# Performance work log

Measured on AMD Instinct MI355X. Metric: run time of the kernel, lower is better.

The kernel has to match this reference:

```python
import jax, jax.numpy as jnp
import numpy as np

T, C, H, W, CI = 4, 64, 96, 96, 16
PS, WS, STR0 = 7, 21, 4
KS, KA = 100, 100
SCALE = 10.0


def conv1x1(x, w, b):
    # x: [T,C,H,W], w: [O,C]
    return jnp.einsum('tchw,oc->tohw', x, w) + b[None, :, None, None]


def unfold_clip(x, ps):
    # clipped-boundary unfold: [T,C,H,W] -> [T, H*W, C*ps*ps]
    t, c, h, w = x.shape
    d = jnp.arange(ps)
    ii = jnp.clip(jnp.arange(h)[:, None] + d[None, :], 0, h - 1)  # [H,ps]
    jj = jnp.clip(jnp.arange(w)[:, None] + d[None, :], 0, w - 1)  # [W,ps]
    p = x[:, :, ii]            # [T,C,H,ps,W]
    p = p[:, :, :, :, jj]      # [T,C,H,ps,W,ps]
    p = jnp.transpose(p, (0, 2, 4, 1, 3, 5))  # [T,H,W,C,ps,ps]
    return p.reshape(t, h * w, c * ps * ps)


def setup_inputs() -> dict:
    key = jax.random.key(0)
    ks = jax.random.split(key, 9)
    s = lambda fan: 1.0 / np.sqrt(fan)
    return {
        'vid': jax.random.normal(ks[0], (T, C, H, W), jnp.float32),
        'g_w': jax.random.normal(ks[1], (CI, C), jnp.float32) * s(C),
        'g_b': jax.random.normal(ks[2], (CI,), jnp.float32) * 0.01,
        'theta_w': jax.random.normal(ks[3], (CI, C), jnp.float32) * s(C),
        'theta_b': jax.random.normal(ks[4], (CI,), jnp.float32) * 0.01,
        'phi_w': jax.random.normal(ks[5], (CI, C), jnp.float32) * s(C),
        'phi_b': jax.random.normal(ks[6], (CI,), jnp.float32) * 0.01,
        'W_w': jax.random.normal(ks[7], (C, CI), jnp.float32) * s(CI),
        'W_b': jax.random.normal(ks[8], (C,), jnp.float32) * 0.01,
    }


def reference(vid, g_w, g_b, theta_w, theta_b, phi_w, phi_b, W_w, W_b):
    t, c, h, w = vid.shape
    b1 = conv1x1(vid, g_w, g_b)          # query features  (g)
    b2 = conv1x1(vid, theta_w, theta_b)  # value features  (theta)
    b3 = conv1x1(vid, phi_w, phi_b)      # key features    (phi)

    b1u = unfold_clip(b1, PS)  # [T,HW,D]
    b2u = unfold_clip(b2, PS)
    b3u = unfold_clip(b3, PS)

    # query grid (stride0)
    qi, qj = jnp.meshgrid(jnp.arange(0, h, STR0), jnp.arange(0, w, STR0), indexing='ij')
    qi, qj = qi.reshape(-1), qj.reshape(-1)
    nq = qi.shape[0]
    qflat = qi * w + qj
    b1q = b1u[:, qflat]  # [T,nq,D]

    # centered spatial search window (stride1=1), clipped bounds
    off = jnp.arange(WS) - WS // 2
    ci = jnp.clip(qi[:, None] + off[None, :], 0, h - 1)  # [nq,WS]
    cj = jnp.clip(qj[:, None] + off[None, :], 0, w - 1)
    cand = (ci[:, :, None] * w + cj[:, None, :]).reshape(nq, WS * WS)

    # patch inner-product dists, one window offset at a time (memory-lean)
    def score(cidx):  # cidx: [nq]
        return jnp.einsum('tqd,tqd->tq', b1q, b3u[:, cidx])
    dists = jax.lax.map(score, cand.T)           # [WS*WS,T,nq]
    dists = jnp.transpose(dists, (1, 2, 0))      # [T,nq,WS*WS]

    vals, idx = jax.lax.top_k(dists, KS)
    vals, idx = vals[..., :KA], idx[..., :KA]
    yi = jax.nn.softmax(vals * SCALE, axis=-1)   # [T,nq,KA]

    pos = jnp.take_along_axis(jnp.broadcast_to(cand[None], (t,) + cand.shape), idx, axis=-1)
    patches = b2u[jnp.arange(t)[:, None, None], pos]   # [T,nq,KA,D]
    zi = jnp.einsum('tqk,tqkd->tqd', yi, patches)      # [T,nq,D]

    # fold: overlap-add scatter + counts normalization
    zi = zi.reshape(t, nq, CI, PS, PS).transpose(0, 2, 1, 3, 4).reshape(t, CI, nq * PS * PS)
    d = jnp.arange(PS)
    pi = jnp.clip(qi[:, None] + d[None, :], 0, h - 1)
    pj = jnp.clip(qj[:, None] + d[None, :], 0, w - 1)
    pix = (pi[:, :, None] * w + pj[:, None, :]).reshape(-1)
    acc = jnp.zeros((t, CI, h * w), vid.dtype).at[:, :, pix].add(zi)
    Z = jnp.zeros((h * w,), vid.dtype).at[pix].add(1.0)
    y = (acc / Z).reshape(t, CI, h, w)

    return vid + conv1x1(y, W_w, W_b)
```

## Files before the change

kernel.cpp:

```cpp
#include <hip/hip_runtime.h>
#include <hip/hip_bf16.h>
#include <hip/hip_fp16.h>
#include <math.h>

typedef __hip_bfloat16 bf16;
typedef unsigned int u32;
typedef unsigned long long u64;
typedef __attribute__((ext_vector_type(8))) short short8;
typedef __attribute__((ext_vector_type(4))) float float4v;

#define T_   4
#define C_   64
#define H_   96
#define W_   96
#define CI_  16
#define HW_  9216
#define NC_  441
#define K_   100
#define HSEL 0x07060302u
#define LSEL 0x05040100u

__device__ __forceinline__ float ldbf(const void* p, int i) { return __bfloat162float(((const bf16*)p)[i]); }
__device__ __forceinline__ float ldf (const void* p, int i) { return ((const float*)p)[i]; }

__device__ __forceinline__ unsigned short f2bf(float x) {
    union { float f; u32 u; } a; a.f = x;
    u32 r = a.u + 0x7FFF + ((a.u >> 16) & 1);
    return (unsigned short)(r >> 16);
}
__device__ __forceinline__ float bf2f(unsigned short s) {
    union { u32 u; float f; } a; a.u = ((u32)s) << 16;
    return a.f;
}
__device__ __forceinline__ u32 packbf(float x) {
    unsigned short h = f2bf(x);
    unsigned short l = f2bf(x - bf2f(h));
    return ((u32)h << 16) | (u32)l;
}
__device__ __forceinline__ u32 okey(float f) {
    u32 u = __float_as_uint(f);
    return u ^ ((u & 0x80000000u) ? 0xFFFFFFFFu : 0x80000000u);
}
__device__ __forceinline__ float unokey(u32 k) {
    u32 u = (k & 0x80000000u) ? (k ^ 0x80000000u) : ~k;
    return __uint_as_float(u);
}
__device__ __forceinline__ int cntdim(int x) {
    int c = 0;
#pragma unroll
    for (int pp = 0; pp < 7; pp++) {
        int q = x - pp;
        c += (q >= 0 && q <= 92 && ((q & 3) == 0)) ? 1 : 0;
    }
    if (x == 95) c += 3;
    return c;
}

__device__ __forceinline__ int detect_flag(const void* vid, int tid, int* sflag) {
    if (tid < 64) {
        unsigned short w = ((const unsigned short*)vid)[tid * 2];
        int e = (w >> 7) & 0xFF;
        int sane = ((e >= 100 && e <= 140) || ((w & 0x7FFF) == 0)) ? 1 : 0;
#pragma unroll
        for (int off = 1; off < 64; off <<= 1) sane += __shfl_xor(sane, off);
        if (tid == 0) *sflag = (sane >= 48) ? 1 : 0;
    }
    __syncthreads();
    return *sflag;
}

__global__ __launch_bounds__(256) void conv3_k(const void* vid, const void* gw, const void* gb,
                                               const void* tw, const void* tb, const void* pw,
                                               const void* pb,
                                               u32* __restrict__ B1p, __half* __restrict__ B2h,
                                               u32* __restrict__ B3p, float* __restrict__ ACCb)
{
    __shared__ float w[3120];
    __shared__ int sflag;
    int tid = threadIdx.x;
    int isbf = detect_flag(vid, tid, &sflag);
    if (isbf) {
        for (int i = tid; i < 3120; i += 256) {
            float v;
            if (i < 1024) v = ldbf(gw, i);
            else if (i < 2048) v = ldbf(tw, i - 1024);
            else if (i < 3072) v = ldbf(pw, i - 2048);
            else if (i < 3088) v = ldbf(gb, i - 3072);
            else if (i < 3104) v = ldbf(tb, i - 3088);
            else v = ldbf(pb, i - 3104);
            w[i] = v;
        }
    } else {
        for (int i = tid; i < 3120; i += 256) {
            float v;
            if (i < 1024) v = ldf(gw, i);
            else if (i < 2048) v = ldf(tw, i - 1024);
            else if (i < 3072) v = ldf(pw, i - 2048);
            else if (i < 3088) v = ldf(gb, i - 3072);
            else if (i < 3104) v = ldf(tb, i - 3088);
            else v = ldf(pb, i - 3104);
            w[i] = v;
        }
    }
    __syncthreads();

    {
        float4v z = {0.f, 0.f, 0.f, 0.f};
        *(float4v*)(ACCb + (blockIdx.x * 256 + tid) * 4) = z;
    }

    int lane = tid & 63, og = tid >> 6;
    int g0 = blockIdx.x * 64 + lane;
    int t = g0 / HW_, pix = g0 - t * HW_;

    float a1[4], a2[4], a3[4];
#pragma unroll
    for (int k = 0; k < 4; k++) {
        a1[k] = w[3072 + og * 4 + k];
        a2[k] = w[3088 + og * 4 + k];
        a3[k] = w[3104 + og * 4 + k];
    }
    int base = t * C_ * HW_ + pix;
#pragma unroll 16
    for (int c = 0; c < C_; c++) {
        float v = isbf ? ldbf(vid, base + c * HW_) : ldf(vid, base + c * HW_);
#pragma unroll
        for (int k = 0; k < 4; k++) {
            a1[k] += v * w[(og * 4 + k) * 64 + c];
            a2[k] += v * w[1024 + (og * 4 + k) * 64 + c];
            a3[k] += v * w[2048 + (og * 4 + k) * 64 + c];
        }
    }
    int ob = g0 * 16 + og * 4;
    uint4 p1, p3;
    p1.x = packbf(a1[0]); p1.y = packbf(a1[1]); p1.z = packbf(a1[2]); p1.w = packbf(a1[3]);
    p3.x = packbf(a3[0]); p3.y = packbf(a3[1]); p3.z = packbf(a3[2]); p3.w = packbf(a3[3]);
    *(uint4*)(B1p + ob) = p1;
    *(uint4*)(B3p + ob) = p3;
    __half2 h01 = __floats2half2_rn(a2[0], a2[1]);
    __half2 h23 = __floats2half2_rn(a2[2], a2[3]);
    uint2 p2;
    p2.x = *(u32*)&h01; p2.y = *(u32*)&h23;
    *(uint2*)(B2h + ob) = p2;
}

__global__ __launch_bounds__(512, 6) void attn_k(const u32* __restrict__ B1p,
                                                 const __half* __restrict__ B2h,
                                                 const u32* __restrict__ B3p,
                                                 float* __restrict__ ACCb)
{
    __shared__ __align__(16) char SM[51344];
    short* Win  = (short*)SM;
    float* Sc   = (float*)(SM + 32768);
    float* Cb   = (float*)(SM + 39824);
    int*   hist = (int*)(SM + 39824);
    float* yiw  = (float*)(SM + 48016);
    int*   pab  = (int*)(SM + 49616);
    int*   ctl  = (int*)(SM + 51216);

    int tid = threadIdx.x;
    int tile = blockIdx.x, t = blockIdx.y;
    int qy = tile / 12, qx = tile - qy * 12;
    int qi = qy * 8, qj = qx * 8;

    const u32*    B1t = B1p + t * HW_ * 16;
    const __half* B2t = B2h + t * HW_ * 16;
    const u32*    B3t = B3p + t * HW_ * 16;

    int lane = tid & 63, wv = tid >> 6;
    int nn = lane & 15, qsel = nn >> 3, pjn = nn & 7;
    int koff = (lane >> 4) * 8;

    for (int pos = tid; pos < 1024; pos += 512) {
        int row = pos >> 5, col = pos & 31;
        int vr = min(max(qi - 10 + row, 0), 95);
        int vc = min(max(qj - 10 + col, 0), 95);
        const u32* src = B3t + (vr * 96 + vc) * 16;
        uint4 U0 = *(const uint4*)src,       U1 = *(const uint4*)(src + 4);
        uint4 U2 = *(const uint4*)(src + 8), U3 = *(const uint4*)(src + 12);
        uint4 A, B;
        A.x = __builtin_amdgcn_perm(U0.y, U0.x, HSEL);
        A.y = __builtin_amdgcn_perm(U0.w, U0.z, HSEL);
        A.z = __builtin_amdgcn_perm(U1.y, U1.x, HSEL);
        A.w = __builtin_amdgcn_perm(U1.w, U1.z, HSEL);
        B.x = __builtin_amdgcn_perm(U2.y, U2.x, HSEL);
        B.y = __builtin_amdgcn_perm(U2.w, U2.z, HSEL);
        B.z = __builtin_amdgcn_perm(U3.y, U3.x, HSEL);
        B.w = __builtin_amdgcn_perm(U3.w, U3.z, HSEL);
        *(uint4*)(Win + pos * 16)     = A;
        *(uint4*)(Win + pos * 16 + 8) = B;
    }
    __syncthreads();

#pragma unroll 1
    for (int ri = 0; ri < 2; ri++) {
        short8 Bh[4], Bl[4];
        int qiq = qi + 4 * ri, qjq = qj + 4 * qsel;
#pragma unroll
        for (int s = 0; s < 4; s++) {
            int kk0 = s * 32 + koff;
            int pi = kk0 >> 4, c0 = kk0 & 15;
            uint4 U0 = {0, 0, 0, 0}, U1 = {0, 0, 0, 0};
            if (pjn < 7 && pi < 7) {
                const u32* src = B1t + (min(qiq + pi, 95) * 96 + min(qjq + pjn, 95)) * 16 + c0;
                U0 = *(const uint4*)src;
                U1 = *(const uint4*)(src + 4);
            }
            union { uint4 u; short8 s8; } hc, lc;
            hc.u.x = __builtin_amdgcn_perm(U0.y, U0.x, HSEL);
            hc.u.y = __builtin_amdgcn_perm(U0.w, U0.z, HSEL);
            hc.u.z = __builtin_amdgcn_perm(U1.y, U1.x, HSEL);
            hc.u.w = __builtin_amdgcn_perm(U1.w, U1.z, HSEL);
            lc.u.x = __builtin_amdgcn_perm(U0.y, U0.x, LSEL);
            lc.u.y = __builtin_amdgcn_perm(U0.w, U0.z, LSEL);
            lc.u.z = __builtin_amdgcn_perm(U1.y, U1.x, LSEL);
            lc.u.w = __builtin_amdgcn_perm(U1.w, U1.z, LSEL);
            Bh[s] = hc.s8; Bl[s] = lc.s8;
        }
        float* Cw = Cb + wv * 256;
        for (int r = wv; r < 21; r += 8) {
            float psum = 0.f;
            int v = (lane >= 21) ? 1 : 0;
            int b = lane - v * 21;
#pragma unroll
            for (int st = 0; st < 2; st++) {
                float4v acc = {0.f, 0.f, 0.f, 0.f};
#pragma unroll
                for (int s = 0; s < 4; s++) {
                    int arow = 4 * ri + r + 2 * s + (lane >> 5);
                    int aoff = (arow * 32 + st * 16 + nn) * 16 + ((lane >> 4) & 1) * 8;
                    short8 A = *(const short8*)(Win + aoff);
                    acc = __builtin_amdgcn_mfma_f32_16x16x32_bf16(A, Bh[s], acc, 0, 0, 0);
                    acc = __builtin_amdgcn_mfma_f32_16x16x32_bf16(A, Bl[s], acc, 0, 0, 0);
                }
                *(float4v*)(Cw + nn * 16 + (lane >> 4) * 4) = acc;
                if (lane < 42) {
#pragma unroll
                    for (int pj = 0; pj < 7; pj++) {
                        int sp = b + 4 * v + pj;
                        if ((sp >> 4) == st) psum += Cw[(8 * v + pj) * 16 + (sp & 15)];
                    }
                }
            }
            if (lane < 42) Sc[(ri * 2 + v) * 441 + r * 21 + b] = psum;
        }
    }
    __syncthreads();

    for (int pos = tid; pos < 1024; pos += 512) {
        int row = pos >> 5, col = pos & 31;
        int vr = min(max(qi - 10 + row, 0), 95);
        int vc = min(max(qj - 10 + col, 0), 95);
        const u32* src = B3t + (vr * 96 + vc) * 16;
        uint4 U0 = *(const uint4*)src,       U1 = *(const uint4*)(src + 4);
        uint4 U2 = *(const uint4*)(src + 8), U3 = *(const uint4*)(src + 12);
        uint4 A, B;
        A.x = __builtin_amdgcn_perm(U0.y, U0.x, LSEL);
        A.y = __builtin_amdgcn_perm(U0.w, U0.z, LSEL);
        A.z = __builtin_amdgcn_perm(U1.y, U1.x, LSEL);
        A.w = __builtin_amdgcn_perm(U1.w, U1.z, LSEL);
        B.x = __builtin_amdgcn_perm(U2.y, U2.x, LSEL);
        B.y = __builtin_amdgcn_perm(U2.w, U2.z, LSEL);
        B.z = __builtin_amdgcn_perm(U3.y, U3.x, LSEL);
        B.w = __builtin_amdgcn_perm(U3.w, U3.z, LSEL);
        *(uint4*)(Win + pos * 16)     = A;
        *(uint4*)(Win + pos * 16 + 8) = B;
    }
    __syncthreads();

#pragma unroll 1
    for (int ri = 0; ri < 2; ri++) {
        short8 Bh[4];
        int qiq = qi + 4 * ri, qjq = qj + 4 * qsel;
#pragma unroll
        for (int s = 0; s < 4; s++) {
            int kk0 = s * 32 + koff;
            int pi = kk0 >> 4, c0 = kk0 & 15;
            uint4 U0 = {0, 0, 0, 0}, U1 = {0, 0, 0, 0};
            if (pjn < 7 && pi < 7) {
                const u32* src = B1t + (min(qiq + pi, 95) * 96 + min(qjq + pjn, 95)) * 16 + c0;
                U0 = *(const uint4*)src;
                U1 = *(const uint4*)(src + 4);
            }
            union { uint4 u; short8 s8; } hc;
            hc.u.x = __builtin_amdgcn_perm(U0.y, U0.x, HSEL);
            hc.u.y = __builtin_amdgcn_perm(U0.w, U0.z, HSEL);
            hc.u.z = __builtin_amdgcn_perm(U1.y, U1.x, HSEL);
            hc.u.w = __builtin_amdgcn_perm(U1.w, U1.z, HSEL);
            Bh[s] = hc.s8;
        }
        float* Cw = Cb + wv * 256;
        for (int r = wv; r < 21; r += 8) {
            float psum = 0.f;
            int v = (lane >= 21) ? 1 : 0;
            int b = lane - v * 21;
#pragma unroll
            for (int st = 0; st < 2; st++) {
                float4v acc = {0.f, 0.f, 0.f, 0.f};
#pragma unroll
                for (int s = 0; s < 4; s++) {
                    int arow = 4 * ri + r + 2 * s + (lane >> 5);
                    int aoff = (arow * 32 + st * 16 + nn) * 16 + ((lane >> 4) & 1) * 8;
                    short8 A = *(const short8*)(Win + aoff);
                    acc = __builtin_amdgcn_mfma_f32_16x16x32_bf16(A, Bh[s], acc, 0, 0, 0);
                }
                *(float4v*)(Cw + nn * 16 + (lane >> 4) * 4) = acc;
                if (lane < 42) {
#pragma unroll
                    for (int pj = 0; pj < 7; pj++) {
                        int sp = b + 4 * v + pj;
                        if ((sp >> 4) == st) psum += Cw[(8 * v + pj) * 16 + (sp & 15)];
                    }
                }
            }
            if (lane < 42) Sc[(ri * 2 + v) * 441 + r * 21 + b] += psum;
        }
    }
    __syncthreads();

    hist[tid] = 0; hist[512 + tid] = 0;
    if (tid < 32) ctl[tid] = ((tid & 7) == 1) ? K_ : 0;
    __syncthreads();

    int g = wv & 3;
    int ri2 = g >> 1, ci2 = g & 1;
    int qiq = qi + 4 * ri2, qjq = qj + 4 * ci2;
    int alo = max(0, 10 - qiq), ahi = min(20, 105 - qiq);
    int blo = max(0, 10 - qjq), bhi = min(20, 105 - qjq);
    u32 kreg[7]; int ni = 0;
    u32 kmax = 0;
    if (wv < 4) {
        for (int i = lane; i < NC_; i += 64) {
            int aa = i / 21, bb = i - aa * 21;
            int ae = min(max(aa, alo), ahi), be = min(max(bb, blo), bhi);
            u32 k = okey(Sc[g * 441 + ae * 21 + be]);
            kmax = max(kmax, k);
            kreg[ni++] = k;
        }
#pragma unroll
        for (int off = 1; off < 64; off <<= 1) kmax = max(kmax, (u32)__shfl_xor((int)kmax, off));
    }

    for (int ps = 3; ps >= 0; ps--) {
        if (wv < 4 && !ctl[g * 8 + 3]) {
            u32 pref = (u32)ctl[g * 8];
            for (int a = 0; a < ni; a++) {
                u32 k = kreg[a];
                if (ps == 3 || (k >> ((ps + 1) * 8)) == pref)
                    atomicAdd(&hist[g * 256 + ((k >> (ps * 8)) & 255)], 1);
            }
        }
        __syncthreads();
        if (wv < 4 && !ctl[g * 8 + 3]) {
            int4 hv = *(int4*)(hist + g * 256 + lane * 4);
            int local = hv.x + hv.y + hv.z + hv.w;
            int s = local;
#pragma unroll
            for (int off = 1; off < 64; off <<= 1) {
                int tt = __shfl_down(s, off);
                if (lane + off < 64) s += tt;
            }
            int c4 = s - local;
            int c3 = c4 + hv.w, c2 = c3 + hv.z, c1 = c2 + hv.y, c0 = s;
            int need = ctl[g * 8 + 1];
            u32 pf = (u32)ctl[g * 8];
            int cums[5] = {c0, c1, c2, c3, c4};
            int hk[4] = {hv.x, hv.y, hv.z, hv.w};
#pragma unroll
            for (int k = 0; k < 4; k++) {
                if (cums[k] >= need && cums[k + 1] < need) {
                    int newneed = need - cums[k + 1];
                    ctl[g * 8]     = (int)((pf << 8) | (u32)(lane * 4 + k));
                    ctl[g * 8 + 1] = newneed;
                    if (newneed == hk[k] || ps == 0) { ctl[g * 8 + 3] = 1; ctl[g * 8 + 2] = 8 * ps; }
                }
            }
            int4 zz = {0, 0, 0, 0};
            *(int4*)(hist + g * 256 + lane * 4) = zz;
        }
        __syncthreads();
        if (ctl[3] && ctl[11] && ctl[19] && ctl[27]) break;
    }

    if (wv >= 4) return;

    u64 am0, am1;
    {
        u32 theta = (u32)ctl[g * 8];
        int shift = ctl[g * 8 + 2];
        int need  = ctl[g * 8 + 1];
        int base  = K_ - need;
        int a2 = 0;
        for (int i = lane; i < NC_; i += 64) {
            u32 k = kreg[a2++];
            u32 hp = k >> shift;
            int slot = -1;
            if (hp > theta) slot = atomicAdd(&ctl[g * 8 + 4], 1);
            else if (hp == theta) {
                int j = atomicAdd(&ctl[g * 8 + 5], 1);
                if (j < need) slot = base + j;
            }
            if (slot >= 0) {
                int a = i / 21, b = i - a * 21;
                int ae = min(max(a, alo), ahi), be = min(max(b, blo), bhi);
                yiw[g * 100 + slot] = unokey(k);
                pab[g * 100 + slot] = ((ae + 4 * ri2) << 8) | (be + 4 * ci2);
            }
        }
        asm volatile("s_waitcnt lgkmcnt(0)" ::: "memory");
        float m = unokey(kmax);
        float wa  = expf((yiw[g * 100 + lane] - m) * 10.f);
        float wb2 = (lane < 36) ? expf((yiw[g * 100 + 64 + lane] - m) * 10.f) : 0.f;
        float ssum = wa + wb2;
#pragma unroll
        for (int off = 1; off < 64; off <<= 1) ssum += __shfl_xor(ssum, off);
        float inv = 1.f / ssum;
        float wan = wa * inv, wbn = wb2 * inv;
        yiw[g * 100 + lane] = wan;
        if (lane < 36) yiw[g * 100 + 64 + lane] = wbn;
        am0 = __ballot(wan != 0.f);
        am1 = __ballot((lane < 36) && (wbn != 0.f));
        asm volatile("s_waitcnt lgkmcnt(0)" ::: "memory");
    }

    if (lane < 49) {
        int rsel = lane & 1;
        int pi2 = lane / 7, pj2 = lane - pi2 * 7;
        __half2 z[8];
#pragma unroll
        for (int j = 0; j < 8; j++) z[j] = __float2half2_rn(0.f);
#pragma unroll 1
        for (int half = 0; half < 2; half++) {
            u64 mm = half ? am1 : am0;
            int kb = half ? 64 : 0;
            while (mm) {
                int k = kb + (__ffsll(mm) - 1);
                mm &= mm - 1;
                float y = yiw[g * 100 + k];
                int pp = pab[g * 100 + k];
                int row = (pp >> 8) + pi2, col = (pp & 255) + pj2;
                int vr = min(max(qi - 10 + row, 0), 95);
                int vc = min(max(qj - 10 + col, 0), 95);
                const __half* cell = B2t + (vr * 96 + vc) * 16;
                int4 A0 = *(const int4*)(cell + rsel * 8);
                int4 A1 = *(const int4*)(cell + 8 - rsel * 8);
                const __half2* pa  = (const __half2*)&A0;
                const __half2* pb2 = (const __half2*)&A1;
                __half2 yh = __float2half2_rn(y);
#pragma unroll
                for (int j = 0; j < 4; j++) {
                    z[j]     = __hfma2(pa[j],  yh, z[j]);
                    z[4 + j] = __hfma2(pb2[j], yh, z[4 + j]);
                }
            }
        }
        int orow = min(qiq + pi2, 95), ocol = min(qjq + pj2, 95);
        float* dst = ACCb + t * CI_ * HW_ + orow * 96 + ocol;
        int c0 = rsel * 8, c1 = 8 - c0;
#pragma unroll
        for (int jh = 0; jh < 4; jh++) {
            atomicAdd(dst + (c0 + 2 * jh) * HW_,     __low2float(z[jh]));
            atomicAdd(dst + (c0 + 2 * jh + 1) * HW_, __high2float(z[jh]));
            atomicAdd(dst + (c1 + 2 * jh) * HW_,     __low2float(z[4 + jh]));
            atomicAdd(dst + (c1 + 2 * jh + 1) * HW_, __high2float(z[4 + jh]));
        }
    }
}

__global__ __launch_bounds__(256) void out_k(const void* vid, const void* Ww, const void* Wb,
                                             const float* __restrict__ ACCb, void* out)
{
    __shared__ float w[1088];
    __shared__ int sflag;
    int tid = threadIdx.x;
    int isbf = detect_flag(vid, tid, &sflag);
    if (isbf) { for (int i = tid; i < 1088; i += 256) w[i] = (i < 1024) ? ldbf(Ww, i) : ldbf(Wb, i - 1024); }
    else      { for (int i = tid; i < 1088; i += 256) w[i] = (i < 1024) ? ldf (Ww, i) : ldf (Wb, i - 1024); }
    __syncthreads();

    int lane5 = tid & 31, oct = tid >> 5;
    int g0 = blockIdx.x * 32 + lane5;
    int t = g0 / HW_, pix = g0 - t * HW_;
    int pi = pix / 96, pj = pix - pi * 96;
    float invz = 1.f / (float)(cntdim(pi) * cntdim(pj));

    float y[CI_];
    int ab = t * CI_ * HW_ + pix;
#pragma unroll
    for (int ci = 0; ci < CI_; ci++) y[ci] = ACCb[ab + ci * HW_] * invz;

    int vb = t * C_ * HW_ + pix;
#pragma unroll
    for (int co = oct * 8; co < oct * 8 + 8; co++) {
        float s = w[1024 + co];
#pragma unroll
        for (int ci = 0; ci < CI_; ci++) s += w[co * 16 + ci] * y[ci];
        int idx = vb + co * HW_;
        float vv = isbf ? ldbf(vid, idx) : ldf(vid, idx);
        float r = vv + s;
        if (isbf) ((bf16*)out)[idx] = __float2bfloat16(r);
        else      ((float*)out)[idx] = r;
    }
}

extern "C" void kernel_launch(void* const* d_in, const int* in_sizes, int n_in,
                              void* d_out, int out_size, void* d_ws, size_t ws_size,
                              hipStream_t stream)
{
    char* ws = (char*)d_ws;
    u32*    B1p  = (u32*)ws;
    __half* B2h  = (__half*)(ws + 2359296);
    u32*    B3p  = (u32*)(ws + 3538944);
    float*  ACCb = (float*)(ws + 5898240);

    conv3_k<<<dim3(576), dim3(256), 0, stream>>>(d_in[0], d_in[1], d_in[2], d_in[3], d_in[4],
                                                 d_in[5], d_in[6], B1p, B2h, B3p, ACCb);
    attn_k<<<dim3(144, T_), dim3(512), 0, stream>>>(B1p, B2h, B3p, ACCb);
    out_k<<<dim3(1152), dim3(256), 0, stream>>>(d_in[0], d_in[7], d_in[8], ACCb, d_out);
}
```

Baseline: 169.9 us.

## Stage value window in LDS with idle waves and drop block barriers in top-k

Waves 4-7, idle during top-k selection, now load the clipped 31x32 fp16 value-feature window into shared memory, reusing the region that held the bf16 score window. Meanwhile waves 0-3 run the radix select with per-wave waitcnt fences in place of block-wide __syncthreads. Each wave owns its own hist/ctl slice, and each one breaks out of the loop independently. The aggregation loop then reads value patches from LDS instead of global memory. The intent is to overlap the global load with selection and to cut barrier and global-gather latency. The change relies on intra-wave LDS ordering being enough, since each group's data is touched only by its own wave.

Result: faster. 164.9 us (-2.9%).

```diff
diff --git a/kernel.cpp b/kernel.cpp
--- a/kernel.cpp
+++ b/kernel.cpp
@@ -150,13 +150,14 @@
                                                  float* __restrict__ ACCb)
 {
     __shared__ __align__(16) char SM[51344];
-    short* Win  = (short*)SM;
-    float* Sc   = (float*)(SM + 32768);
-    float* Cb   = (float*)(SM + 39824);
-    int*   hist = (int*)(SM + 39824);
-    float* yiw  = (float*)(SM + 48016);
-    int*   pab  = (int*)(SM + 49616);
-    int*   ctl  = (int*)(SM + 51216);
+    short*   Win  = (short*)SM;
+    __half2* Wp   = (__half2*)SM;
+    float*   Sc   = (float*)(SM + 32768);
+    float*   Cb   = (float*)(SM + 39824);
+    int*     hist = (int*)(SM + 39824);
+    float*   yiw  = (float*)(SM + 48016);
+    int*     pab  = (int*)(SM + 49616);
+    int*     ctl  = (int*)(SM + 51216);
 
     int tid = threadIdx.x;
     int tile = blockIdx.x, t = blockIdx.y;
@@ -318,18 +319,25 @@
     }
     __syncthreads();
 
-    hist[tid] = 0; hist[512 + tid] = 0;
-    if (tid < 32) ctl[tid] = ((tid & 7) == 1) ? K_ : 0;
-    __syncthreads();
-
     int g = wv & 3;
     int ri2 = g >> 1, ci2 = g & 1;
     int qiq = qi + 4 * ri2, qjq = qj + 4 * ci2;
     int alo = max(0, 10 - qiq), ahi = min(20, 105 - qiq);
     int blo = max(0, 10 - qjq), bhi = min(20, 105 - qjq);
-    u32 kreg[7]; int ni = 0;
-    u32 kmax = 0;
-    if (wv < 4) {
+    u64 am0 = 0, am1 = 0;
+
+    if (wv >= 4) {
+        for (int pos = tid - 256; pos < 992; pos += 256) {
+            int row = pos >> 5, col = pos & 31;
+            int vr = min(max(qi - 10 + row, 0), 95);
+            int vc = min(max(qj - 10 + col, 0), 95);
+            const __half* src = B2t + (vr * 96 + vc) * 16;
+            *(int4*)(Wp + pos * 8)     = *(const int4*)src;
+            *(int4*)(Wp + pos * 8 + 4) = *(const int4*)(src + 8);
+        }
+    } else {
+        u32 kreg[7]; int ni = 0;
+        u32 kmax = 0;
         for (int i = lane; i < NC_; i += 64) {
             int aa = i / 21, bb = i - aa * 21;
             int ae = min(max(aa, alo), ahi), be = min(max(bb, blo), bhi);
@@ -339,19 +347,24 @@
         }
 #pragma unroll
         for (int off = 1; off < 64; off <<= 1) kmax = max(kmax, (u32)__shfl_xor((int)kmax, off));
-    }
-
-    for (int ps = 3; ps >= 0; ps--) {
-        if (wv < 4 && !ctl[g * 8 + 3]) {
-            u32 pref = (u32)ctl[g * 8];
+
+        {
+            int4 zz = {0, 0, 0, 0};
+            *(int4*)(hist + g * 256 + lane * 4) = zz;
+            if (lane < 8) ctl[g * 8 + lane] = (lane == 1) ? K_ : 0;
+        }
+        asm volatile("s_waitcnt lgkmcnt(0)" ::: "memory");
+
+#pragma unroll 1
+        for (int ps = 3; ps >= 0; ps--) {
+            u32 pref  = (u32)ctl[g * 8];
+            int need0 = ctl[g * 8 + 1];
             for (int a = 0; a < ni; a++) {
                 u32 k = kreg[a];
                 if (ps == 3 || (k >> ((ps + 1) * 8)) == pref)
                     atomicAdd(&hist[g * 256 + ((k >> (ps * 8)) & 255)], 1);
             }
-        }
-        __syncthreads();
-        if (wv < 4 && !ctl[g * 8 + 3]) {
+            asm volatile("s_waitcnt lgkmcnt(0)" ::: "memory");
             int4 hv = *(int4*)(hist + g * 256 + lane * 4);
             int local = hv.x + hv.y + hv.z + hv.w;
             int s = local;
@@ -362,66 +375,63 @@
             }
             int c4 = s - local;
             int c3 = c4 + hv.w, c2 = c3 + hv.z, c1 = c2 + hv.y, c0 = s;
-            int need = ctl[g * 8 + 1];
-            u32 pf = (u32)ctl[g * 8];
             int cums[5] = {c0, c1, c2, c3, c4};
             int hk[4] = {hv.x, hv.y, hv.z, hv.w};
 #pragma unroll
             for (int k = 0; k < 4; k++) {
-                if (cums[k] >= need && cums[k + 1] < need) {
-                    int newneed = need - cums[k + 1];
-                    ctl[g * 8]     = (int)((pf << 8) | (u32)(lane * 4 + k));
+                if (cums[k] >= need0 && cums[k + 1] < need0) {
+                    int newneed = need0 - cums[k + 1];
+                    ctl[g * 8]     = (int)((pref << 8) | (u32)(lane * 4 + k));
                     ctl[g * 8 + 1] = newneed;
                     if (newneed == hk[k] || ps == 0) { ctl[g * 8 + 3] = 1; ctl[g * 8 + 2] = 8 * ps; }
                 }
             }
             int4 zz = {0, 0, 0, 0};
             *(int4*)(hist + g * 256 + lane * 4) = zz;
-        }
-        __syncthreads();
-        if (ctl[3] && ctl[11] && ctl[19] && ctl[27]) break;
-    }
-
+            asm volatile("s_waitcnt lgkmcnt(0)" ::: "memory");
+            if (ctl[g * 8 + 3]) break;
+        }
+
+        {
+            u32 theta = (u32)ctl[g * 8];
+            int shift = ctl[g * 8 + 2];
+            int need  = ctl[g * 8 + 1];
+            int base  = K_ - need;
+            int a2 = 0;
+            for (int i = lane; i < NC_; i += 64) {
+                u32 k = kreg[a2++];
+                u32 hp = k >> shift;
+                int slot = -1;
+                if (hp > theta) slot = atomicAdd(&ctl[g * 8 + 4], 1);
+                else if (hp == theta) {
+                    int j = atomicAdd(&ctl[g * 8 + 5], 1);
+                    if (j < need) slot = base + j;
+                }
+                if (slot >= 0) {
+                    int a = i / 21, b = i - a * 21;
+                    int ae = min(max(a, alo), ahi), be = min(max(b, blo), bhi);
+                    yiw[g * 100 + slot] = unokey(k);
+                    pab[g * 100 + slot] = ((ae + 4 * ri2) << 8) | (be + 4 * ci2);
+                }
+            }
+            asm volatile("s_waitcnt lgkmcnt(0)" ::: "memory");
+            float m = unokey(kmax);
+            float wa  = expf((yiw[g * 100 + lane] - m) * 10.f);
+            float wb2 = (lane < 36) ? expf((yiw[g * 100 + 64 + lane] - m) * 10.f) : 0.f;
+            float ssum = wa + wb2;
+#pragma unroll
+            for (int off = 1; off < 64; off <<= 1) ssum += __shfl_xor(ssum, off);
+            float inv = 1.f / ssum;
+            float wan = wa * inv, wbn = wb2 * inv;
+            yiw[g * 100 + lane] = wan;
+            if (lane < 36) yiw[g * 100 + 64 + lane] = wbn;
+            am0 = __ballot(wan != 0.f);
+            am1 = __ballot((lane < 36) && (wbn != 0.f));
+            asm volatile("s_waitcnt lgkmcnt(0)" ::: "memory");
+        }
+    }
+    __syncthreads();
     if (wv >= 4) return;
-
-    u64 am0, am1;
-    {
-        u32 theta = (u32)ctl[g * 8];
-        int shift = ctl[g * 8 + 2];
-        int need  = ctl[g * 8 + 1];
-        int base  = K_ - need;
-        int a2 = 0;
-        for (int i = lane; i < NC_; i += 64) {
-            u32 k = kreg[a2++];
-            u32 hp = k >> shift;
-            int slot = -1;
-            if (hp > theta) slot = atomicAdd(&ctl[g * 8 + 4], 1);
-            else if (hp == theta) {
-                int j = atomicAdd(&ctl[g * 8 + 5], 1);
-                if (j < need) slot = base + j;
-            }
-            if (slot >= 0) {
-                int a = i / 21, b = i - a * 21;
-                int ae = min(max(a, alo), ahi), be = min(max(b, blo), bhi);
-                yiw[g * 100 + slot] = unokey(k);
-                pab[g * 100 + slot] = ((ae + 4 * ri2) << 8) | (be + 4 * ci2);
-            }
-        }
-        asm volatile("s_waitcnt lgkmcnt(0)" ::: "memory");
-        float m = unokey(kmax);
-        float wa  = expf((yiw[g * 100 + lane] - m) * 10.f);
-        float wb2 = (lane < 36) ? expf((yiw[g * 100 + 64 + lane] - m) * 10.f) : 0.f;
-        float ssum = wa + wb2;
-#pragma unroll
-        for (int off = 1; off < 64; off <<= 1) ssum += __shfl_xor(ssum, off);
-        float inv = 1.f / ssum;
-        float wan = wa * inv, wbn = wb2 * inv;
-        yiw[g * 100 + lane] = wan;
-        if (lane < 36) yiw[g * 100 + 64 + lane] = wbn;
-        am0 = __ballot(wan != 0.f);
-        am1 = __ballot((lane < 36) && (wbn != 0.f));
-        asm volatile("s_waitcnt lgkmcnt(0)" ::: "memory");
-    }
 
     if (lane < 49) {
         int rsel = lane & 1;
@@ -439,11 +449,9 @@
                 float y = yiw[g * 100 + k];
                 int pp = pab[g * 100 + k];
                 int row = (pp >> 8) + pi2, col = (pp & 255) + pj2;
-                int vr = min(max(qi - 10 + row, 0), 95);
-                int vc = min(max(qj - 10 + col, 0), 95);
-                const __half* cell = B2t + (vr * 96 + vc) * 16;
-                int4 A0 = *(const int4*)(cell + rsel * 8);
-                int4 A1 = *(const int4*)(cell + 8 - rsel * 8);
+                const __half2* cell = Wp + (row * 32 + col) * 8;
+                int4 A0 = *(const int4*)(cell + rsel * 4);
+                int4 A1 = *(const int4*)(cell + 4 - rsel * 4);
                 const __half2* pa  = (const __half2*)&A0;
                 const __half2* pb2 = (const __half2*)&A1;
                 __half2 yh = __float2half2_rn(y);
```
